# Kernel optimization log

Measured on AMD Instinct MI355X. Metric: run time of the kernel, lower is better.

Reference implementation:

```python
import jax, jax.numpy as jnp
import numpy as np

B, P, N, C = 4, 12, 1024, 64  # batch, past window, nodes, channels (in==hidden==out)


def setup_inputs() -> dict:
    key = jax.random.key(0)
    k1, k2, k3, k4, k5, k6 = jax.random.split(key, 6)
    x = jax.random.normal(k1, (B, P, N, C), dtype=jnp.float32)
    # float adjacency mask in {0,1}; force self-loops so no softmax row is empty
    A = jax.random.randint(k2, (B, P, N, N), 0, 2).astype(jnp.float32)
    A = A.at[..., jnp.arange(N), jnp.arange(N)].set(1.0)
    # learned params (nn.Linear stores weight as [out, in]; y = x @ W.T)
    W_emb = jax.random.normal(k3, (C, C), dtype=jnp.float32) / jnp.sqrt(jnp.float32(C))
    a1 = jax.random.normal(k4, (C,), dtype=jnp.float32)
    a2 = jax.random.normal(k5, (C,), dtype=jnp.float32)
    W_lin = jax.random.normal(k6, (C, C), dtype=jnp.float32) / jnp.sqrt(jnp.float32(C))
    return {"x": x, "A": A, "W_emb": W_emb, "a1": a1, "a2": a2, "W_lin": W_lin}


def reference(x, A, W_emb, a1, a2, W_lin):
    # x_emb = emb(x)  (bias-free linear)
    x_emb = jnp.einsum('bpnc,hc->bpnh', x, W_emb)            # [B,P,N,H]
    s1 = x_emb @ a1                                           # [B,P,N]
    s2 = x_emb @ a2                                           # [B,P,N]
    # additive GAT scores: a1_i + a2_j, broadcast instead of repeat
    z = jax.nn.leaky_relu(s1[..., :, None] + s2[..., None, :], 0.01)  # [B,P,N,N]
    z = jnp.where(A == 0.0, -jnp.inf, z)
    pi = jax.nn.softmax(z, axis=-1)                           # masked attention
    agg = jnp.einsum('bpij,bpjc->bpic', pi, x)                # weighted aggregation
    out = jax.nn.sigmoid(jnp.einsum('bpic,oc->bpio', agg, W_lin))
    return (out, A)
```

## Files before the change

kernel.cpp:

```cpp
#include <hip/hip_runtime.h>

typedef __attribute__((ext_vector_type(8))) __bf16 bf16x8;
typedef __attribute__((ext_vector_type(4))) float f32x4;

#define N_ 1024
#define C_ 64
#define BP_ 48

static __device__ __forceinline__ unsigned short f2bf(float f) {
    __bf16 b = (__bf16)f;
    return __builtin_bit_cast(unsigned short, b);
}
static __device__ __forceinline__ unsigned int pack2(float a, float b) {
    return (unsigned int)f2bf(a) | ((unsigned int)f2bf(b) << 16);
}
static __device__ __forceinline__ void load_lds16(const float* g, float* s) {
    __builtin_amdgcn_global_load_lds(
        (__attribute__((address_space(1))) void*)(void*)g,
        (__attribute__((address_space(3))) void*)s, 16, 0, 0);
}

__global__ __launch_bounds__(256) void gat_pre(
    const float* __restrict__ x, const float* __restrict__ Wemb,
    const float* __restrict__ a1, const float* __restrict__ a2,
    float* __restrict__ s1g, float* __restrict__ s2g,
    unsigned short* __restrict__ xT, float* __restrict__ M2part)
{
    __shared__ float xs[64][65];
    __shared__ float vs[2][64];
    const int t = threadIdx.x, l = t & 63, w = t >> 6;
    const int j0 = blockIdx.x * 64;
    const int bp = blockIdx.y;

    if (w == 0) {
        float v1 = 0.f, v2 = 0.f;
        #pragma unroll 8
        for (int h = 0; h < 64; ++h) {
            float we = Wemb[h * 64 + l];
            v1 = fmaf(a1[h], we, v1);
            v2 = fmaf(a2[h], we, v2);
        }
        vs[0][l] = v1; vs[1][l] = v2;
    }
    const float* xb = x + ((size_t)bp * N_ + j0) * C_;
    #pragma unroll
    for (int it = 0; it < 16; ++it)
        xs[it * 4 + w][l] = xb[(it * 4 + w) * C_ + l];
    __syncthreads();

    const int jr = t >> 2, c0 = (t & 3) * 16;
    float p1 = 0.f, p2 = 0.f;
    #pragma unroll
    for (int k = 0; k < 16; ++k) {
        float xv = xs[jr][c0 + k];
        p1 = fmaf(xv, vs[0][c0 + k], p1);
        p2 = fmaf(xv, vs[1][c0 + k], p2);
    }
    p1 += __shfl_xor(p1, 1); p1 += __shfl_xor(p1, 2);
    p2 += __shfl_xor(p2, 1); p2 += __shfl_xor(p2, 2);
    if ((l & 3) == 0) {
        s1g[bp * N_ + j0 + jr] = p1;
        s2g[bp * N_ + j0 + jr] = p2;
    }
    float m = p2;
    m = fmaxf(m, __shfl_xor(m, 4));
    m = fmaxf(m, __shfl_xor(m, 8));
    m = fmaxf(m, __shfl_xor(m, 16));
    m = fmaxf(m, __shfl_xor(m, 32));
    if (l == 0) M2part[bp * 64 + blockIdx.x * 4 + w] = m;

    const int c = t >> 2, part = t & 3;
    unsigned int ow[8];
    #pragma unroll
    for (int k = 0; k < 16; k += 2) {
        unsigned int lo = f2bf(xs[part * 16 + k][c]);
        unsigned int hi = f2bf(xs[part * 16 + k + 1][c]);
        ow[k >> 1] = lo | (hi << 16);
    }
    uint4* dst = (uint4*)(xT + (size_t)bp * C_ * N_ + (size_t)c * N_ + j0 + part * 16);
    dst[0] = make_uint4(ow[0], ow[1], ow[2], ow[3]);
    dst[1] = make_uint4(ow[4], ow[5], ow[6], ow[7]);
}

__global__ __launch_bounds__(256) void gat_fused(
    const float* __restrict__ Ag, float* __restrict__ outA,
    const unsigned short* __restrict__ xT,
    const float* __restrict__ s1g, const float* __restrict__ s2g,
    const float* __restrict__ M2part,
    const float* __restrict__ Wlin, float* __restrict__ out)
{
    __shared__ float ldsA[4][2][1024];
    __shared__ unsigned short Plds[4][16][72];
    __shared__ float s2lds[1024];
    __shared__ float lsLDS[4][16];

    const int t = threadIdx.x, l = t & 63, w = t >> 6;
    const int i15 = l & 15, q = l >> 4;
    const int lm = l & 15, g16 = l >> 4;
    const int bp = blockIdx.y;
    const int ibase = blockIdx.x * 64 + w * 16;

    *(f32x4*)&s2lds[4 * t] = *(const f32x4*)&s2g[bp * N_ + 4 * t];

    float m2v = M2part[bp * 64 + l];
    #pragma unroll
    for (int off = 32; off >= 1; off >>= 1)
        m2v = fmaxf(m2v, __shfl_xor(m2v, off));
    const float M2 = m2v;
    const float s1_l = s1g[bp * N_ + ibase + i15];

    __syncthreads();

    const float* Arow = Ag + (size_t)bp * N_ * N_ + (size_t)ibase * N_;
    float* oArow = outA + (size_t)bp * N_ * N_ + (size_t)ibase * N_;
    const unsigned short* xTb = xT + (size_t)bp * C_ * N_;

    f32x4 acc[4] = {};
    float ls4[4] = {0.f, 0.f, 0.f, 0.f};

    #pragma unroll
    for (int r4 = 0; r4 < 4; ++r4)
        load_lds16(&Arow[(size_t)(4 * r4 + g16) * N_ + 4 * lm],
                   &ldsA[w][0][r4 * 256]);

    for (int k = 0; k < 16; ++k) {
        asm volatile("s_waitcnt vmcnt(0)" ::: "memory");
        const int cb = k & 1;
        const int j0c = k * 64;
        if (k < 15) {
            #pragma unroll
            for (int r4 = 0; r4 < 4; ++r4)
                load_lds16(&Arow[(size_t)(4 * r4 + g16) * N_ + j0c + 64 + 4 * lm],
                           &ldsA[w][cb ^ 1][r4 * 256]);
        }
        const f32x4 s2v = *(const f32x4*)&s2lds[j0c + 4 * lm];
        #pragma unroll
        for (int sr = 0; sr < 4; ++sr) {
            f32x4 Av = *(const f32x4*)&ldsA[w][cb][sr * 256 + 4 * l];
            *(f32x4*)&oArow[(size_t)(4 * sr + g16) * N_ + j0c + 4 * lm] = Av;
            float s1v = __shfl(s1_l, 4 * sr + g16);
            float zr = s1v + M2;
            float mv = fmaxf(zr, 0.01f * zr);
            float e[4];
            #pragma unroll
            for (int kk = 0; kk < 4; ++kk) {
                float zz = s1v + s2v[kk];
                zz = fmaxf(zz, 0.01f * zz);
                e[kk] = (Av[kk] != 0.f) ? __expf(zz - mv) : 0.f;
            }
            ls4[sr] += (e[0] + e[1]) + (e[2] + e[3]);
            *(uint2*)&Plds[w][4 * sr + g16][4 * lm] =
                make_uint2(pack2(e[0], e[1]), pack2(e[2], e[3]));
        }
        #pragma unroll
        for (int s = 0; s < 2; ++s) {
            bf16x8 af = *(const bf16x8*)&Plds[w][i15][s * 32 + q * 8];
            #pragma unroll
            for (int nt = 0; nt < 4; ++nt) {
                bf16x8 bfr = *(const bf16x8*)&xTb[(size_t)(nt * 16 + i15) * N_ +
                                                  j0c + s * 32 + q * 8];
                acc[nt] = __builtin_amdgcn_mfma_f32_16x16x32_bf16(af, bfr, acc[nt], 0, 0, 0);
            }
        }
    }

    #pragma unroll
    for (int sr = 0; sr < 4; ++sr) {
        ls4[sr] += __shfl_xor(ls4[sr], 1);
        ls4[sr] += __shfl_xor(ls4[sr], 2);
        ls4[sr] += __shfl_xor(ls4[sr], 4);
        ls4[sr] += __shfl_xor(ls4[sr], 8);
    }
    if (lm == 0) {
        #pragma unroll
        for (int sr = 0; sr < 4; ++sr)
            lsLDS[w][4 * sr + g16] = ls4[sr];
    }
    const f32x4 lsq = *(const f32x4*)&lsLDS[w][4 * q];

    unsigned short* aggl = &Plds[w][0][0];
    #pragma unroll
    for (int nt = 0; nt < 4; ++nt)
        #pragma unroll
        for (int r = 0; r < 4; ++r)
            aggl[(q * 4 + r) * 72 + nt * 16 + i15] = f2bf(acc[nt][r] / lsq[r]);

    f32x4 d2[4] = {};
    #pragma unroll
    for (int s = 0; s < 2; ++s) {
        bf16x8 af = *(const bf16x8*)&aggl[i15 * 72 + s * 32 + q * 8];
        #pragma unroll
        for (int nt = 0; nt < 4; ++nt) {
            const float* wp = Wlin + (size_t)(nt * 16 + i15) * C_ + s * 32 + q * 8;
            f32x4 w0 = *(const f32x4*)wp;
            f32x4 w1 = *(const f32x4*)(wp + 4);
            bf16x8 bfr;
            #pragma unroll
            for (int jj = 0; jj < 4; ++jj) { bfr[jj] = (__bf16)w0[jj]; bfr[4 + jj] = (__bf16)w1[jj]; }
            d2[nt] = __builtin_amdgcn_mfma_f32_16x16x32_bf16(af, bfr, d2[nt], 0, 0, 0);
        }
    }
    float* orow = out + ((size_t)bp * N_ + ibase) * C_;
    #pragma unroll
    for (int nt = 0; nt < 4; ++nt)
        #pragma unroll
        for (int r = 0; r < 4; ++r)
            orow[(size_t)(q * 4 + r) * C_ + nt * 16 + i15] =
                1.f / (1.f + __expf(-d2[nt][r]));
}

extern "C" void kernel_launch(void* const* d_in, const int* in_sizes, int n_in,
                              void* d_out, int out_size, void* d_ws, size_t ws_size,
                              hipStream_t stream) {
    const float* x    = (const float*)d_in[0];
    const float* Ag   = (const float*)d_in[1];
    const float* Wemb = (const float*)d_in[2];
    const float* a1   = (const float*)d_in[3];
    const float* a2   = (const float*)d_in[4];
    const float* Wlin = (const float*)d_in[5];
    float* out  = (float*)d_out;
    float* outA = out + (size_t)BP_ * N_ * C_;

    float* s1g = (float*)d_ws;
    float* s2g = s1g + BP_ * N_;
    float* M2part = s2g + BP_ * N_;
    unsigned short* xT = (unsigned short*)(M2part + BP_ * 64);

    gat_pre<<<dim3(16, BP_), dim3(256), 0, stream>>>(x, Wemb, a1, a2,
                                                     s1g, s2g, xT, M2part);
    gat_fused<<<dim3(16, BP_), dim3(256), 0, stream>>>(Ag, outA, xT, s1g, s2g,
                                                       M2part, Wlin, out);
}
```

Baseline: 399.0 us.

## Prefetch adjacency tiles into registers instead of LDS double buffer

Replaces the global_load_lds double buffer for the adjacency chunks with direct register loads, ping-ponged across two register sets in a manually unrolled loop. This drops the 32 KB LDS buffer and the per-iteration vmcnt(0) wait, and adds a launch-bounds occupancy hint of 4 blocks. The per-row s1 shuffle and max computation are hoisted out of the loop. The cost is higher register pressure, and the loads can no longer complete asynchronously into LDS.

```diff
diff --git a/kernel.cpp b/kernel.cpp
--- a/kernel.cpp
+++ b/kernel.cpp
@@ -13,11 +13,6 @@
 }
 static __device__ __forceinline__ unsigned int pack2(float a, float b) {
     return (unsigned int)f2bf(a) | ((unsigned int)f2bf(b) << 16);
-}
-static __device__ __forceinline__ void load_lds16(const float* g, float* s) {
-    __builtin_amdgcn_global_load_lds(
-        (__attribute__((address_space(1))) void*)(void*)g,
-        (__attribute__((address_space(3))) void*)s, 16, 0, 0);
 }
 
 __global__ __launch_bounds__(256) void gat_pre(
@@ -82,14 +77,13 @@
     dst[1] = make_uint4(ow[4], ow[5], ow[6], ow[7]);
 }
 
-__global__ __launch_bounds__(256) void gat_fused(
+__global__ __launch_bounds__(256, 4) void gat_fused(
     const float* __restrict__ Ag, float* __restrict__ outA,
     const unsigned short* __restrict__ xT,
     const float* __restrict__ s1g, const float* __restrict__ s2g,
     const float* __restrict__ M2part,
     const float* __restrict__ Wlin, float* __restrict__ out)
 {
-    __shared__ float ldsA[4][2][1024];
     __shared__ unsigned short Plds[4][16][72];
     __shared__ float s2lds[1024];
     __shared__ float lsLDS[4][16];
@@ -109,60 +103,75 @@
     const float M2 = m2v;
     const float s1_l = s1g[bp * N_ + ibase + i15];
 
+    float s1r[4], mvr[4];
+    #pragma unroll
+    for (int sr = 0; sr < 4; ++sr) {
+        s1r[sr] = __shfl(s1_l, 4 * sr + g16);
+        float zr = s1r[sr] + M2;
+        mvr[sr] = fmaxf(zr, 0.01f * zr);
+    }
+
     __syncthreads();
 
-    const float* Arow = Ag + (size_t)bp * N_ * N_ + (size_t)ibase * N_;
-    float* oArow = outA + (size_t)bp * N_ * N_ + (size_t)ibase * N_;
+    const float* Arow = Ag + ((size_t)bp * N_ + ibase + g16) * N_ + 4 * lm;
+    float* oArow = outA + ((size_t)bp * N_ + ibase + g16) * N_ + 4 * lm;
     const unsigned short* xTb = xT + (size_t)bp * C_ * N_;
 
     f32x4 acc[4] = {};
     float ls4[4] = {0.f, 0.f, 0.f, 0.f};
 
-    #pragma unroll
-    for (int r4 = 0; r4 < 4; ++r4)
-        load_lds16(&Arow[(size_t)(4 * r4 + g16) * N_ + 4 * lm],
-                   &ldsA[w][0][r4 * 256]);
-
-    for (int k = 0; k < 16; ++k) {
-        asm volatile("s_waitcnt vmcnt(0)" ::: "memory");
-        const int cb = k & 1;
-        const int j0c = k * 64;
-        if (k < 15) {
-            #pragma unroll
-            for (int r4 = 0; r4 < 4; ++r4)
-                load_lds16(&Arow[(size_t)(4 * r4 + g16) * N_ + j0c + 64 + 4 * lm],
-                           &ldsA[w][cb ^ 1][r4 * 256]);
-        }
-        const f32x4 s2v = *(const f32x4*)&s2lds[j0c + 4 * lm];
-        #pragma unroll
-        for (int sr = 0; sr < 4; ++sr) {
-            f32x4 Av = *(const f32x4*)&ldsA[w][cb][sr * 256 + 4 * l];
-            *(f32x4*)&oArow[(size_t)(4 * sr + g16) * N_ + j0c + 4 * lm] = Av;
-            float s1v = __shfl(s1_l, 4 * sr + g16);
-            float zr = s1v + M2;
-            float mv = fmaxf(zr, 0.01f * zr);
-            float e[4];
-            #pragma unroll
-            for (int kk = 0; kk < 4; ++kk) {
-                float zz = s1v + s2v[kk];
-                zz = fmaxf(zz, 0.01f * zz);
-                e[kk] = (Av[kk] != 0.f) ? __expf(zz - mv) : 0.f;
-            }
-            ls4[sr] += (e[0] + e[1]) + (e[2] + e[3]);
-            *(uint2*)&Plds[w][4 * sr + g16][4 * lm] =
-                make_uint2(pack2(e[0], e[1]), pack2(e[2], e[3]));
-        }
-        #pragma unroll
-        for (int s = 0; s < 2; ++s) {
-            bf16x8 af = *(const bf16x8*)&Plds[w][i15][s * 32 + q * 8];
-            #pragma unroll
-            for (int nt = 0; nt < 4; ++nt) {
-                bf16x8 bfr = *(const bf16x8*)&xTb[(size_t)(nt * 16 + i15) * N_ +
-                                                  j0c + s * 32 + q * 8];
-                acc[nt] = __builtin_amdgcn_mfma_f32_16x16x32_bf16(af, bfr, acc[nt], 0, 0, 0);
-            }
-        }
-    }
+    f32x4 Aa0, Aa1, Aa2, Aa3, Ab0, Ab1, Ab2, Ab3;
+
+#define LOADA(d0, d1, d2, d3, kk) do {                                        \
+    const float* _p = Arow + (kk) * 64;                                       \
+    d0 = *(const f32x4*)(_p);                                                 \
+    d1 = *(const f32x4*)(_p + 4 * N_);                                        \
+    d2 = *(const f32x4*)(_p + 8 * N_);                                        \
+    d3 = *(const f32x4*)(_p + 12 * N_); } while (0)
+
+#define DOSR(Av, sr, j0c) do {                                                \
+    *(f32x4*)(oArow + (sr) * 4 * N_ + (j0c)) = Av;                            \
+    float e0, e1, e2, e3;                                                     \
+    { float zz = s1r[sr] + s2v[0]; zz = fmaxf(zz, 0.01f * zz);                \
+      e0 = (Av[0] != 0.f) ? __expf(zz - mvr[sr]) : 0.f; }                     \
+    { float zz = s1r[sr] + s2v[1]; zz = fmaxf(zz, 0.01f * zz);                \
+      e1 = (Av[1] != 0.f) ? __expf(zz - mvr[sr]) : 0.f; }                     \
+    { float zz = s1r[sr] + s2v[2]; zz = fmaxf(zz, 0.01f * zz);                \
+      e2 = (Av[2] != 0.f) ? __expf(zz - mvr[sr]) : 0.f; }                     \
+    { float zz = s1r[sr] + s2v[3]; zz = fmaxf(zz, 0.01f * zz);                \
+      e3 = (Av[3] != 0.f) ? __expf(zz - mvr[sr]) : 0.f; }                     \
+    ls4[sr] += (e0 + e1) + (e2 + e3);                                         \
+    *(uint2*)&Plds[w][4 * (sr) + g16][4 * lm] =                               \
+        make_uint2(pack2(e0, e1), pack2(e2, e3)); } while (0)
+
+#define CONSUME(a0, a1, a2, a3, kk) do {                                      \
+    const int j0c = (kk) * 64;                                                \
+    const f32x4 s2v = *(const f32x4*)&s2lds[j0c + 4 * lm];                    \
+    DOSR(a0, 0, j0c); DOSR(a1, 1, j0c); DOSR(a2, 2, j0c); DOSR(a3, 3, j0c);  \
+    _Pragma("unroll")                                                         \
+    for (int s = 0; s < 2; ++s) {                                             \
+        bf16x8 af = *(const bf16x8*)&Plds[w][i15][s * 32 + q * 8];            \
+        _Pragma("unroll")                                                     \
+        for (int nt = 0; nt < 4; ++nt) {                                      \
+            bf16x8 bfr = *(const bf16x8*)&xTb[(size_t)(nt * 16 + i15) * N_ +  \
+                                              j0c + s * 32 + q * 8];          \
+            acc[nt] = __builtin_amdgcn_mfma_f32_16x16x32_bf16(af, bfr,        \
+                                                              acc[nt], 0, 0, 0); \
+        }                                                                     \
+    } } while (0)
+
+    LOADA(Aa0, Aa1, Aa2, Aa3, 0);
+    #pragma unroll 1
+    for (int k = 0; k < 16; k += 2) {
+        LOADA(Ab0, Ab1, Ab2, Ab3, k + 1);
+        CONSUME(Aa0, Aa1, Aa2, Aa3, k);
+        if (k + 2 < 16)
+            LOADA(Aa0, Aa1, Aa2, Aa3, k + 2);
+        CONSUME(Ab0, Ab1, Ab2, Ab3, k + 1);
+    }
+#undef LOADA
+#undef DOSR
+#undef CONSUME
 
     #pragma unroll
     for (int sr = 0; sr < 4; ++sr) {
```

Measured after the change: 403.5 us. Within noise of the previous version (+1.1%).
